# Performance work log

Measured on AMD Instinct MI355X. Metric: run time of the kernel, lower is better.

Reference implementation:

```python
import jax, jax.numpy as jnp
import numpy as np

EMBED_DIM = 1024
NUM_HEADS = 16
D_K = EMBED_DIM // NUM_HEADS


def setup_inputs() -> dict:
    key = jax.random.key(0)
    ks = jax.random.split(key, 5)
    s = 1.0 / np.sqrt(EMBED_DIM)  # roughly match nn.Linear init scale
    return {
        "x": jax.random.normal(ks[0], (2, 2048, EMBED_DIM), dtype=jnp.float32),
        "wq": jax.random.normal(ks[1], (EMBED_DIM, EMBED_DIM), dtype=jnp.float32) * s,
        "wk": jax.random.normal(ks[2], (EMBED_DIM, EMBED_DIM), dtype=jnp.float32) * s,
        "wv": jax.random.normal(ks[3], (EMBED_DIM, EMBED_DIM), dtype=jnp.float32) * s,
        "wo": jax.random.normal(ks[4], (EMBED_DIM, EMBED_DIM), dtype=jnp.float32) * s,
    }


def reference(x, wq, wk, wv, wo):
    b, s, e = x.shape
    # nn.Linear(bias=False): y = x @ W.T
    def split_heads(t):
        return t.reshape(b, s, NUM_HEADS, D_K).transpose(0, 2, 1, 3)  # [b,h,s,d]
    q = split_heads(x @ wq.T)
    k = split_heads(x @ wk.T)
    v = split_heads(x @ wv.T)
    scores = jnp.einsum("bhqd,bhkd->bhqk", q, k) / jnp.sqrt(jnp.float32(D_K))
    attn = jax.nn.softmax(scores, axis=-1)
    out = jnp.einsum("bhqk,bhkd->bhqd", attn, v)  # [b,h,s,d]
    out = out.transpose(0, 2, 1, 3).reshape(b, s, e)
    return out @ wo.T
```

## Files before the change

### kernel.cpp

```cpp
#include <hip/hip_runtime.h>
#include <stdint.h>

typedef unsigned short u16;
typedef float f32x4 __attribute__((ext_vector_type(4)));
typedef __bf16 bf16x8 __attribute__((ext_vector_type(8)));
typedef short s16x4 __attribute__((ext_vector_type(4)));

__device__ __forceinline__ u16 f2bf(float f) {
  union { float f; uint32_t u; } c; c.f = f;
  uint32_t u = c.u;
  u += 0x7fffu + ((u >> 16) & 1u);
  return (u16)(u >> 16);
}

__device__ __forceinline__ uint32_t pkbf(float a, float b) {
  union { float f; uint32_t u; } ua, ub; ua.f = a; ub.f = b;
  return __builtin_amdgcn_perm(ub.u, ua.u, 0x07060302u);
}

#define GLOAD_LDS16(g, l)                                                              \
  __builtin_amdgcn_global_load_lds((__attribute__((address_space(1))) void*)(g),       \
                                   (__attribute__((address_space(3))) void*)(l), 16, 0, 0)

__global__ __launch_bounds__(256) void cvt_all(const float* __restrict__ x,
                                               const float* __restrict__ wq,
                                               const float* __restrict__ wk,
                                               const float* __restrict__ wv,
                                               const float* __restrict__ wo,
                                               u16* __restrict__ xb,
                                               u16* __restrict__ wqkvb,
                                               u16* __restrict__ wob) {
  int bx = blockIdx.x;
  const float* src;
  u16* dst;
  int i;
  if (bx < 4096) {
    src = x; dst = xb; i = bx * 256 + threadIdx.x;
  } else {
    int r = bx - 4096;
    int w = r >> 10;
    i = (r & 1023) * 256 + threadIdx.x;
    if (w == 0)      { src = wq; dst = wqkvb; }
    else if (w == 1) { src = wk; dst = wqkvb + 1048576; }
    else if (w == 2) { src = wv; dst = wqkvb + 2097152; }
    else             { src = wo; dst = wob; }
  }
  const float4 v = ((const float4*)src)[i];
  ushort4 o;
  o.x = f2bf(v.x); o.y = f2bf(v.y); o.z = f2bf(v.z); o.w = f2bf(v.w);
  ((ushort4*)dst)[i] = o;
}

__global__ __launch_bounds__(256) void gemm_qkv(const u16* __restrict__ A,
                                                const u16* __restrict__ B,
                                                u16* __restrict__ QKb,
                                                u16* __restrict__ Vt) {
  const int K = 1024;
  __shared__ __align__(16) u16 sA[128 * 64];
  __shared__ __align__(16) u16 sB[128 * 64];
  const int tid = threadIdx.x;
  const int lane = tid & 63;
  const int wave = tid >> 6;
  const int quad = lane >> 4, l16 = lane & 15;
  const int wm = (wave >> 1) * 64, wn = (wave & 1) * 64;
  const int bm = blockIdx.y * 128, bn = blockIdx.x * 128;

  f32x4 acc[4][4];
#pragma unroll
  for (int i = 0; i < 4; i++)
#pragma unroll
    for (int j = 0; j < 4; j++) acc[i][j] = (f32x4){0.f, 0.f, 0.f, 0.f};

  for (int k0 = 0; k0 < K; k0 += 64) {
#pragma unroll
    for (int k2 = 0; k2 < 4; k2++) {
      int c = k2 * 256 + tid;
      int row = c >> 3, c8 = (c & 7) ^ (row & 7);
      GLOAD_LDS16(A + (size_t)(bm + row) * K + k0 + c8 * 8, (char*)sA + c * 16);
      GLOAD_LDS16(B + (size_t)(bn + row) * K + k0 + c8 * 8, (char*)sB + c * 16);
    }
    __syncthreads();
    bf16x8 af[4][2], bfr[4][2];
#pragma unroll
    for (int mt = 0; mt < 4; mt++)
#pragma unroll
      for (int kh = 0; kh < 2; kh++) {
        int ra = wm + mt * 16 + l16;
        af[mt][kh] = *(const bf16x8*)&sA[ra * 64 + (((kh * 4 + quad) ^ (ra & 7)) * 8)];
        int rb = wn + mt * 16 + l16;
        bfr[mt][kh] = *(const bf16x8*)&sB[rb * 64 + (((kh * 4 + quad) ^ (rb & 7)) * 8)];
      }
#pragma unroll
    for (int mt = 0; mt < 4; mt++)
#pragma unroll
      for (int nt = 0; nt < 4; nt++) {
        acc[mt][nt] = __builtin_amdgcn_mfma_f32_16x16x32_bf16(af[mt][0], bfr[nt][0], acc[mt][nt], 0, 0, 0);
        acc[mt][nt] = __builtin_amdgcn_mfma_f32_16x16x32_bf16(af[mt][1], bfr[nt][1], acc[mt][nt], 0, 0, 0);
      }
    __syncthreads();
  }

  if (blockIdx.x < 16) {
    const float qs = (blockIdx.x < 8) ? 0.18033688011f : 1.0f;
#pragma unroll
    for (int mt = 0; mt < 4; mt++)
#pragma unroll
      for (int nt = 0; nt < 4; nt++)
#pragma unroll
        for (int r = 0; r < 4; r++) {
          int row = bm + wm + mt * 16 + quad * 4 + r;
          int col = bn + wn + nt * 16 + l16;
          QKb[(size_t)row * 2048 + col] = f2bf(acc[mt][nt][r] * qs);
        }
  } else {
#pragma unroll
    for (int mt = 0; mt < 4; mt++)
#pragma unroll
      for (int nt = 0; nt < 4; nt++) {
        int hd = (bn - 2048) + wn + nt * 16 + l16;
        int tok = bm + wm + mt * 16 + quad * 4;
        ushort4 o;
        o.x = f2bf(acc[mt][nt][0]);
        o.y = f2bf(acc[mt][nt][1]);
        o.z = f2bf(acc[mt][nt][2]);
        o.w = f2bf(acc[mt][nt][3]);
        *(ushort4*)&Vt[(size_t)hd * 4096 + tok] = o;
      }
  }
}

__global__ __launch_bounds__(256, 4) void attn_fwd(const u16* __restrict__ QKb,
                                                   const u16* __restrict__ Vt,
                                                   u16* __restrict__ O) {
  const int bx = blockIdx.x;
  const int qt = bx >> 5;
  const int h  = (bx >> 1) & 15;
  const int b  = bx & 1;
  const int tid = threadIdx.x;
  const int lane = tid & 63;
  const int wave = tid >> 6;
  const int quad = lane >> 4, l16 = lane & 15;

  __shared__ __align__(16) u16 smem[20480];
  u16* sK0 = smem;
  u16* sK1 = smem + 4096;
  u16* sV0 = smem + 8192;
  u16* sV1 = smem + 12288;
  u16* sQ  = smem + 16384;

  const int tok0 = b * 2048;
  const int q0 = qt * 64;
  const int colh = h * 64;

#pragma unroll
  for (int k2 = 0; k2 < 2; k2++) {
    int c = k2 * 256 + tid;
    int row = c >> 3, c8 = (c & 7) ^ (row & 7);
    GLOAD_LDS16(QKb + (size_t)(tok0 + q0 + row) * 2048 + colh + c8 * 8,
                (char*)sQ + c * 16);
  }
#pragma unroll
  for (int k2 = 0; k2 < 2; k2++) {
    int c = k2 * 256 + tid;
    int row = c >> 3, c8 = (c & 7) ^ (row & 7);
    GLOAD_LDS16(QKb + (size_t)(tok0 + row) * 2048 + 1024 + colh + c8 * 8,
                (char*)sK0 + c * 16);
    GLOAD_LDS16(Vt + (size_t)(colh + row) * 4096 + tok0 + c8 * 8,
                (char*)sV0 + c * 16);
  }
  __syncthreads();

  bf16x8 aq[2];
#pragma unroll
  for (int kh = 0; kh < 2; kh++) {
    int row = wave * 16 + l16;
    aq[kh] = *(const bf16x8*)&sQ[row * 64 + (((kh * 4 + quad) ^ (row & 7)) * 8)];
  }

  f32x4 oacc[4];
  float lsum = 0.f;
#pragma unroll
  for (int db = 0; db < 4; db++) oacc[db] = (f32x4){0.f, 0.f, 0.f, 0.f};

  int p = 0;
  for (int it = 0; it < 32; ++it) {
    u16* sKc = p ? sK1 : sK0;
    u16* sVc = p ? sV1 : sV0;
    if (it < 31) {
      u16* sKn = p ? sK0 : sK1;
      u16* sVn = p ? sV0 : sV1;
      const int nkv = (it + 1) * 64;
#pragma unroll
      for (int k2 = 0; k2 < 2; k2++) {
        int c = k2 * 256 + tid;
        int row = c >> 3, c8 = (c & 7) ^ (row & 7);
        GLOAD_LDS16(QKb + (size_t)(tok0 + nkv + row) * 2048 + 1024 + colh + c8 * 8,
                    (char*)sKn + c * 16);
        GLOAD_LDS16(Vt + (size_t)(colh + row) * 4096 + tok0 + nkv + c8 * 8,
                    (char*)sVn + c * 16);
      }
    }

    bf16x8 kf[4][2];
#pragma unroll
    for (int nt = 0; nt < 4; nt++)
#pragma unroll
      for (int kh = 0; kh < 2; kh++) {
        int rr = nt * 16 + l16;
        kf[nt][kh] = *(const bf16x8*)&sKc[rr * 64 + (((kh * 4 + quad) ^ (rr & 7)) * 8)];
      }
    s16x4 vf[4][4];
#pragma unroll
    for (int db = 0; db < 4; db++)
#pragma unroll
      for (int nt = 0; nt < 4; nt++) {
        int row = db * 16 + l16;
        int c16 = (nt * 2 + (quad >> 1)) ^ (row & 7);
        vf[db][nt] = *(const s16x4*)&sVc[row * 64 + c16 * 8 + (quad & 1) * 4];
      }

    float e[4][4];
#pragma unroll
    for (int nt = 0; nt < 4; nt++) {
      f32x4 c = (f32x4){0.f, 0.f, 0.f, 0.f};
      c = __builtin_amdgcn_mfma_f32_16x16x32_bf16(kf[nt][0], aq[0], c, 0, 0, 0);
      c = __builtin_amdgcn_mfma_f32_16x16x32_bf16(kf[nt][1], aq[1], c, 0, 0, 0);
#pragma unroll
      for (int r = 0; r < 4; r++) e[nt][r] = __builtin_amdgcn_exp2f(c[r]);
      lsum += (e[nt][0] + e[nt][1]) + (e[nt][2] + e[nt][3]);
    }
#pragma unroll
    for (int nt = 0; nt < 4; nt++) {
      union { uint32_t u[2]; s16x4 v; } bb;
      bb.u[0] = pkbf(e[nt][0], e[nt][1]);
      bb.u[1] = pkbf(e[nt][2], e[nt][3]);
#pragma unroll
      for (int db = 0; db < 4; db++)
        oacc[db] = __builtin_amdgcn_mfma_f32_16x16x16bf16_1k(vf[db][nt], bb.v, oacc[db], 0, 0, 0);
    }
    __syncthreads();
    p ^= 1;
  }

  {
    float v = lsum;
    v += __shfl_xor(v, 16, 64);
    v += __shfl_xor(v, 32, 64);
    lsum = 1.0f / v;
  }

  u16* sT = smem + wave * 1088;
#pragma unroll
  for (int db = 0; db < 4; db++)
#pragma unroll
    for (int r = 0; r < 4; r++)
      sT[l16 * 68 + db * 16 + quad * 4 + r] = f2bf(oacc[db][r] * lsum);
#pragma unroll
  for (int k = 0; k < 2; k++) {
    int qrow = k * 8 + (lane >> 3);
    int cch = lane & 7;
    uint4 vrow = *(const uint4*)&sT[qrow * 68 + cch * 8];
    int tokr = tok0 + q0 + wave * 16 + qrow;
    *(uint4*)&O[(size_t)tokr * 1024 + colh + cch * 8] = vrow;
  }
}

__global__ __launch_bounds__(256) void gemm_out(const u16* __restrict__ A,
                                                const u16* __restrict__ B,
                                                float* __restrict__ C) {
  const int N = 1024, K = 1024;
  __shared__ __align__(16) u16 sA[128 * 64];
  __shared__ __align__(16) u16 sB[64 * 64];
  const int tid = threadIdx.x;
  const int lane = tid & 63;
  const int wave = tid >> 6;
  const int quad = lane >> 4, l16 = lane & 15;
  const int wm = (wave >> 1) * 64, wn = (wave & 1) * 32;
  const int bm = blockIdx.y * 128, bn = blockIdx.x * 64;

  f32x4 acc[4][2];
#pragma unroll
  for (int i = 0; i < 4; i++)
#pragma unroll
    for (int j = 0; j < 2; j++) acc[i][j] = (f32x4){0.f, 0.f, 0.f, 0.f};

  for (int k0 = 0; k0 < K; k0 += 64) {
#pragma unroll
    for (int k2 = 0; k2 < 4; k2++) {
      int c = k2 * 256 + tid;
      int row = c >> 3, c8 = (c & 7) ^ (row & 7);
      GLOAD_LDS16(A + (size_t)(bm + row) * K + k0 + c8 * 8, (char*)sA + c * 16);
    }
#pragma unroll
    for (int k2 = 0; k2 < 2; k2++) {
      int c = k2 * 256 + tid;
      int row = c >> 3, c8 = (c & 7) ^ (row & 7);
      GLOAD_LDS16(B + (size_t)(bn + row) * K + k0 + c8 * 8, (char*)sB + c * 16);
    }
    __syncthreads();
    bf16x8 af[4][2], bfr[2][2];
#pragma unroll
    for (int mt = 0; mt < 4; mt++)
#pragma unroll
      for (int kh = 0; kh < 2; kh++) {
        int ra = wm + mt * 16 + l16;
        af[mt][kh] = *(const bf16x8*)&sA[ra * 64 + (((kh * 4 + quad) ^ (ra & 7)) * 8)];
      }
#pragma unroll
    for (int nt = 0; nt < 2; nt++)
#pragma unroll
      for (int kh = 0; kh < 2; kh++) {
        int rb = wn + nt * 16 + l16;
        bfr[nt][kh] = *(const bf16x8*)&sB[rb * 64 + (((kh * 4 + quad) ^ (rb & 7)) * 8)];
      }
#pragma unroll
    for (int mt = 0; mt < 4; mt++)
#pragma unroll
      for (int nt = 0; nt < 2; nt++) {
        acc[mt][nt] = __builtin_amdgcn_mfma_f32_16x16x32_bf16(af[mt][0], bfr[nt][0], acc[mt][nt], 0, 0, 0);
        acc[mt][nt] = __builtin_amdgcn_mfma_f32_16x16x32_bf16(af[mt][1], bfr[nt][1], acc[mt][nt], 0, 0, 0);
      }
    __syncthreads();
  }

#pragma unroll
  for (int mt = 0; mt < 4; mt++)
#pragma unroll
    for (int nt = 0; nt < 2; nt++)
#pragma unroll
      for (int r = 0; r < 4; r++) {
        int row = bm + wm + mt * 16 + quad * 4 + r;
        int col = bn + wn + nt * 16 + l16;
        C[(size_t)row * N + col] = acc[mt][nt][r];
      }
}

extern "C" void kernel_launch(void* const* d_in, const int* in_sizes, int n_in,
                              void* d_out, int out_size, void* d_ws, size_t ws_size,
                              hipStream_t stream) {
  const float* x  = (const float*)d_in[0];
  const float* wq = (const float*)d_in[1];
  const float* wk = (const float*)d_in[2];
  const float* wv = (const float*)d_in[3];
  const float* wo = (const float*)d_in[4];
  float* out = (float*)d_out;
  char* ws = (char*)d_ws;
  const size_t MB = 1u << 20;

  u16* xb    = (u16*)(ws);
  u16* wqkvb = (u16*)(ws + 8 * MB);
  u16* wob   = (u16*)(ws + 14 * MB);
  u16* QKb   = (u16*)(ws + 16 * MB);
  u16* Vtb   = (u16*)(ws + 32 * MB);
  u16* Ob    = xb;

  cvt_all<<<8192, 256, 0, stream>>>(x, wq, wk, wv, wo, xb, wqkvb, wob);

  gemm_qkv<<<dim3(24, 32), 256, 0, stream>>>(xb, wqkvb, QKb, Vtb);

  attn_fwd<<<1024, 256, 0, stream>>>(QKb, Vtb, Ob);

  gemm_out<<<dim3(16, 32), 256, 0, stream>>>(Ob, wob, out);
}
```

Before: 192.1 us.

## Use two-wave attention blocks with each wave handling 32 query rows

```diff
diff --git a/kernel.cpp b/kernel.cpp
--- a/kernel.cpp
+++ b/kernel.cpp
@@ -129,7 +129,7 @@
   }
 }
 
-__global__ __launch_bounds__(256, 4) void attn_fwd(const u16* __restrict__ QKb,
+__global__ __launch_bounds__(128, 2) void attn_fwd(const u16* __restrict__ QKb,
                                                    const u16* __restrict__ Vt,
                                                    u16* __restrict__ O) {
   const int bx = blockIdx.x;
@@ -153,15 +153,15 @@
   const int colh = h * 64;
 
 #pragma unroll
-  for (int k2 = 0; k2 < 2; k2++) {
-    int c = k2 * 256 + tid;
+  for (int k2 = 0; k2 < 4; k2++) {
+    int c = k2 * 128 + tid;
     int row = c >> 3, c8 = (c & 7) ^ (row & 7);
     GLOAD_LDS16(QKb + (size_t)(tok0 + q0 + row) * 2048 + colh + c8 * 8,
                 (char*)sQ + c * 16);
   }
 #pragma unroll
-  for (int k2 = 0; k2 < 2; k2++) {
-    int c = k2 * 256 + tid;
+  for (int k2 = 0; k2 < 4; k2++) {
+    int c = k2 * 128 + tid;
     int row = c >> 3, c8 = (c & 7) ^ (row & 7);
     GLOAD_LDS16(QKb + (size_t)(tok0 + row) * 2048 + 1024 + colh + c8 * 8,
                 (char*)sK0 + c * 16);
@@ -170,17 +170,21 @@
   }
   __syncthreads();
 
-  bf16x8 aq[2];
-#pragma unroll
-  for (int kh = 0; kh < 2; kh++) {
-    int row = wave * 16 + l16;
-    aq[kh] = *(const bf16x8*)&sQ[row * 64 + (((kh * 4 + quad) ^ (row & 7)) * 8)];
-  }
-
-  f32x4 oacc[4];
-  float lsum = 0.f;
-#pragma unroll
-  for (int db = 0; db < 4; db++) oacc[db] = (f32x4){0.f, 0.f, 0.f, 0.f};
+  bf16x8 aq[2][2];
+#pragma unroll
+  for (int sub = 0; sub < 2; sub++)
+#pragma unroll
+    for (int kh = 0; kh < 2; kh++) {
+      int row = wave * 32 + sub * 16 + l16;
+      aq[sub][kh] = *(const bf16x8*)&sQ[row * 64 + (((kh * 4 + quad) ^ (row & 7)) * 8)];
+    }
+
+  f32x4 oacc[2][4];
+  float lsum[2] = {0.f, 0.f};
+#pragma unroll
+  for (int sub = 0; sub < 2; sub++)
+#pragma unroll
+    for (int db = 0; db < 4; db++) oacc[sub][db] = (f32x4){0.f, 0.f, 0.f, 0.f};
 
   int p = 0;
   for (int it = 0; it < 32; ++it) {
@@ -191,8 +195,8 @@
       u16* sVn = p ? sV0 : sV1;
       const int nkv = (it + 1) * 64;
 #pragma unroll
-      for (int k2 = 0; k2 < 2; k2++) {
-        int c = k2 * 256 + tid;
+      for (int k2 = 0; k2 < 4; k2++) {
+        int c = k2 * 128 + tid;
         int row = c >> 3, c8 = (c & 7) ^ (row & 7);
         GLOAD_LDS16(QKb + (size_t)(tok0 + nkv + row) * 2048 + 1024 + colh + c8 * 8,
                     (char*)sKn + c * 16);
@@ -219,48 +223,54 @@
         vf[db][nt] = *(const s16x4*)&sVc[row * 64 + c16 * 8 + (quad & 1) * 4];
       }
 
-    float e[4][4];
-#pragma unroll
-    for (int nt = 0; nt < 4; nt++) {
-      f32x4 c = (f32x4){0.f, 0.f, 0.f, 0.f};
-      c = __builtin_amdgcn_mfma_f32_16x16x32_bf16(kf[nt][0], aq[0], c, 0, 0, 0);
-      c = __builtin_amdgcn_mfma_f32_16x16x32_bf16(kf[nt][1], aq[1], c, 0, 0, 0);
-#pragma unroll
-      for (int r = 0; r < 4; r++) e[nt][r] = __builtin_amdgcn_exp2f(c[r]);
-      lsum += (e[nt][0] + e[nt][1]) + (e[nt][2] + e[nt][3]);
-    }
-#pragma unroll
-    for (int nt = 0; nt < 4; nt++) {
-      union { uint32_t u[2]; s16x4 v; } bb;
-      bb.u[0] = pkbf(e[nt][0], e[nt][1]);
-      bb.u[1] = pkbf(e[nt][2], e[nt][3]);
-#pragma unroll
-      for (int db = 0; db < 4; db++)
-        oacc[db] = __builtin_amdgcn_mfma_f32_16x16x16bf16_1k(vf[db][nt], bb.v, oacc[db], 0, 0, 0);
+#pragma unroll
+    for (int sub = 0; sub < 2; sub++) {
+      float e[4][4];
+#pragma unroll
+      for (int nt = 0; nt < 4; nt++) {
+        f32x4 c = (f32x4){0.f, 0.f, 0.f, 0.f};
+        c = __builtin_amdgcn_mfma_f32_16x16x32_bf16(kf[nt][0], aq[sub][0], c, 0, 0, 0);
+        c = __builtin_amdgcn_mfma_f32_16x16x32_bf16(kf[nt][1], aq[sub][1], c, 0, 0, 0);
+#pragma unroll
+        for (int r = 0; r < 4; r++) e[nt][r] = __builtin_amdgcn_exp2f(c[r]);
+        lsum[sub] += (e[nt][0] + e[nt][1]) + (e[nt][2] + e[nt][3]);
+      }
+#pragma unroll
+      for (int nt = 0; nt < 4; nt++) {
+        union { uint32_t u[2]; s16x4 v; } bb;
+        bb.u[0] = pkbf(e[nt][0], e[nt][1]);
+        bb.u[1] = pkbf(e[nt][2], e[nt][3]);
+#pragma unroll
+        for (int db = 0; db < 4; db++)
+          oacc[sub][db] = __builtin_amdgcn_mfma_f32_16x16x16bf16_1k(vf[db][nt], bb.v, oacc[sub][db], 0, 0, 0);
+      }
     }
     __syncthreads();
     p ^= 1;
   }
 
-  {
-    float v = lsum;
+#pragma unroll
+  for (int sub = 0; sub < 2; sub++) {
+    float v = lsum[sub];
     v += __shfl_xor(v, 16, 64);
     v += __shfl_xor(v, 32, 64);
-    lsum = 1.0f / v;
-  }
-
-  u16* sT = smem + wave * 1088;
-#pragma unroll
-  for (int db = 0; db < 4; db++)
-#pragma unroll
-    for (int r = 0; r < 4; r++)
-      sT[l16 * 68 + db * 16 + quad * 4 + r] = f2bf(oacc[db][r] * lsum);
-#pragma unroll
-  for (int k = 0; k < 2; k++) {
+    lsum[sub] = 1.0f / v;
+  }
+
+  u16* sT = smem + wave * 2176;
+#pragma unroll
+  for (int sub = 0; sub < 2; sub++)
+#pragma unroll
+    for (int db = 0; db < 4; db++)
+#pragma unroll
+      for (int r = 0; r < 4; r++)
+        sT[(sub * 16 + l16) * 68 + db * 16 + quad * 4 + r] = f2bf(oacc[sub][db][r] * lsum[sub]);
+#pragma unroll
+  for (int k = 0; k < 4; k++) {
     int qrow = k * 8 + (lane >> 3);
     int cch = lane & 7;
     uint4 vrow = *(const uint4*)&sT[qrow * 68 + cch * 8];
-    int tokr = tok0 + q0 + wave * 16 + qrow;
+    int tokr = tok0 + q0 + wave * 32 + qrow;
     *(uint4*)&O[(size_t)tokr * 1024 + colh + cch * 8] = vrow;
   }
 }
@@ -358,7 +368,7 @@
 
   gemm_qkv<<<dim3(24, 32), 256, 0, stream>>>(xb, wqkvb, QKb, Vtb);
 
-  attn_fwd<<<1024, 256, 0, stream>>>(QKb, Vtb, Ob);
+  attn_fwd<<<1024, 128, 0, stream>>>(QKb, Vtb, Ob);
 
   gemm_out<<<dim3(16, 32), 256, 0, stream>>>(Ob, wob, out);
 }
```

Result: faster. 186.9 us (-2.7%).
